# Optimization experiments

Measured on AMD Instinct MI355X. Metric: run time of the kernel, lower is better.

Reference implementation:

```python
import jax, jax.numpy as jnp
import numpy as np

ALPHA = 4.0  # spikingjelly default Sigmoid surrogate alpha
BN_EPS = 1e-5

@jax.custom_vjp
def spike(x):
    return (x >= 0.0).astype(x.dtype)

def _spike_fwd(x):
    return spike(x), x

def _spike_bwd(res, g):
    s = jax.nn.sigmoid(ALPHA * res)
    return (g * ALPHA * s * (1.0 - s),)

spike.defvjp(_spike_fwd, _spike_bwd)

def lif(x, tau=2.0, vth=1.0):
    # MultiStepLIFNode: hard reset (v_reset=0), detach_reset=True, scan over time axis 0
    def step(v, xt):
        h = v + (xt - v) / tau          # charge
        s = spike(h - vth)              # fire (surrogate grad)
        v_next = h * (1.0 - jax.lax.stop_gradient(s))  # detached hard reset to 0
        return v_next, s
    _, out = jax.lax.scan(step, jnp.zeros_like(x[0]), x)
    return out

def conv_bn(x, w, b, g, be, m, var):
    # x: [TB, C, N]; 1x1 Conv1d is a channel GEMM, then eval-mode BatchNorm1d
    y = jnp.einsum('oc,bcn->bon', w, x) + b[None, :, None]
    inv = g / jnp.sqrt(var + BN_EPS)
    return (y - m[None, :, None]) * inv[None, :, None] + be[None, :, None]

def setup_inputs() -> dict:
    key = jax.random.key(0)
    T, B, C, H, W = 4, 32, 512, 14, 14
    ks = jax.random.split(key, 32)
    d = {'x': jax.random.normal(ks[0], (T, B, C, H, W), dtype=jnp.float32)}
    scale = 1.0 / np.sqrt(C)
    i = 1
    for p in ['q', 'k', 'v', 'p']:
        d[p + '_cw'] = jax.random.normal(ks[i], (C, C), dtype=jnp.float32) * scale; i += 1
        d[p + '_cb'] = jax.random.normal(ks[i], (C,), dtype=jnp.float32) * 0.1; i += 1
        d[p + '_bg'] = jnp.ones((C,), dtype=jnp.float32)
        d[p + '_bb'] = jnp.zeros((C,), dtype=jnp.float32)
        d[p + '_bm'] = jax.random.normal(ks[i], (C,), dtype=jnp.float32) * 0.1; i += 1
        d[p + '_bv'] = jax.random.uniform(ks[i], (C,), dtype=jnp.float32, minval=0.5, maxval=1.5); i += 1
    d['push_w'] = jnp.asarray(1.0, dtype=jnp.float32)
    d['pull_w'] = jnp.asarray(1.0, dtype=jnp.float32)
    d['pp_bias'] = jnp.asarray(0.0, dtype=jnp.float32)
    return d

def reference(x,
              q_cw, q_cb, q_bg, q_bb, q_bm, q_bv,
              k_cw, k_cb, k_bg, k_bb, k_bm, k_bv,
              v_cw, v_cb, v_bg, v_bb, v_bm, v_bv,
              p_cw, p_cb, p_bg, p_bb, p_bm, p_bv,
              push_w, pull_w, pp_bias):
    T, B, C, H, W = x.shape
    N = H * W
    nh = 8
    hd = C // nh
    scale = 0.125

    xs = lif(x)                                   # head_lif, [T,B,C,H,W]
    xf = xs.reshape(T * B, C, N)
    q = conv_bn(xf, q_cw, q_cb, q_bg, q_bb, q_bm, q_bv).reshape(T, B, C, N)
    k = conv_bn(xf, k_cw, k_cb, k_bg, k_bb, k_bm, k_bv).reshape(T, B, C, N)
    v = conv_bn(xf, v_cw, v_cb, v_bg, v_bb, v_bm, v_bv).reshape(T, B, C, N)

    q_on = lif(q)
    q_off = lif(-q)

    def to_heads(t):  # [T,B,C,N] -> [T,B,nh,N,hd]
        return jnp.swapaxes(t, -1, -2).reshape(T, B, N, nh, hd).transpose(0, 1, 3, 2, 4)

    q_on_h = to_heads(q_on)
    q_off_h = to_heads(q_off)
    k_h = to_heads(lif(k))
    v_h = to_heads(lif(v))

    pw = jax.nn.softplus(push_w)
    pl = jax.nn.softplus(pull_w)
    diff = pw * q_on_h - pl * q_off_h + pp_bias   # push-pull gating
    q_pp = lif(diff)

    kv = jnp.einsum('tbhnd,tbhne->tbhde', k_h, v_h)      # k^T @ v, [T,B,h,hd,hd]
    o = jnp.einsum('tbhnd,tbhde->tbhne', q_pp, kv) * scale

    o = o.transpose(0, 1, 2, 4, 3).reshape(T, B, C, N)   # transpose(3,4) then merge heads
    o = lif(o, vth=0.5)                                   # attn_lif
    o = conv_bn(o.reshape(T * B, C, N), p_cw, p_cb, p_bg, p_bb, p_bm, p_bv)
    return o.reshape(T, B, C, H, W)
```

## Files before the change

### kernel.cpp

```cpp
#include <hip/hip_runtime.h>
#include <hip/hip_bf16.h>
#include <math.h>

typedef unsigned short u16;
typedef unsigned int   u32;

#define CC 512
#define NN 196
#define TT 4
#define BB 32
#define TBB 128
#define NHH 8
#define HD 64

#define ROWS_T  6272
#define CSTRIDE ((size_t)ROWS_T * CC)

typedef __attribute__((ext_vector_type(8))) _Float16 f16x8;
typedef __attribute__((ext_vector_type(4))) float f32x4;

#define ONE_H 0x3C00

__device__ __forceinline__ u16 h_bits(_Float16 h) { return *(u16*)&h; }
__device__ __forceinline__ float h2f(u16 u) { return (float)(*(const _Float16*)&u); }
__device__ __forceinline__ u32 pk2(u16 a, u16 b) { return (u32)a | ((u32)b << 16); }

__device__ __forceinline__ void gld16(const void* g, void* l) {
    __builtin_amdgcn_global_load_lds(
        (const __attribute__((address_space(1))) void*)g,
        (__attribute__((address_space(3))) void*)l, 16, 0, 0);
}

__global__ __launch_bounds__(256) void k_prep(
    const float* __restrict__ qw, const float* __restrict__ kw,
    const float* __restrict__ vw, const float* __restrict__ pw,
    const float* __restrict__ cb0, const float* __restrict__ bg0, const float* __restrict__ bb0,
    const float* __restrict__ bm0, const float* __restrict__ bv0,
    const float* __restrict__ cb1, const float* __restrict__ bg1, const float* __restrict__ bb1,
    const float* __restrict__ bm1, const float* __restrict__ bv1,
    const float* __restrict__ cb2, const float* __restrict__ bg2, const float* __restrict__ bb2,
    const float* __restrict__ bm2, const float* __restrict__ bv2,
    const float* __restrict__ cb3, const float* __restrict__ bg3, const float* __restrict__ bb3,
    const float* __restrict__ bm3, const float* __restrict__ bv3,
    u16* __restrict__ W2, float* __restrict__ SS, float* __restrict__ SH) {
    if (blockIdx.x < 4096) {
        size_t idx = (size_t)blockIdx.x * 256 + threadIdx.x;
        int g = (int)(idx >> 18);
        size_t rem = idx & 262143;
        const float* Ws = (g == 0) ? qw : (g == 1) ? kw : (g == 2) ? vw : pw;
        float w  = Ws[rem];
        _Float16 h0 = (fabsf(w) < 6.2e-5f) ? (_Float16)0.0f : (_Float16)w;
        float r = (w - (float)h0) * 2048.0f;
        _Float16 h1 = (_Float16)r;
        size_t base = (size_t)g * 524288 + rem;
        W2[base] = h_bits(h0); W2[base + 262144] = h_bits(h1);
        return;
    }
    int idx = (blockIdx.x - 4096) * 256 + threadIdx.x;
    int g = idx >> 9, o = idx & 511;
    const float* cb = g == 0 ? cb0 : g == 1 ? cb1 : g == 2 ? cb2 : cb3;
    const float* bg = g == 0 ? bg0 : g == 1 ? bg1 : g == 2 ? bg2 : bg3;
    const float* bb = g == 0 ? bb0 : g == 1 ? bb1 : g == 2 ? bb2 : bb3;
    const float* bm = g == 0 ? bm0 : g == 1 ? bm1 : g == 2 ? bm2 : bm3;
    const float* bv = g == 0 ? bv0 : g == 1 ? bv1 : g == 2 ? bv2 : bv3;
    float inv = bg[o] / sqrtf(bv[o] + 1e-5f);
    SS[g * 512 + o] = inv;
    SH[g * 512 + o] = (cb[o] - bm[o]) * inv + bb[o];
}

__global__ __launch_bounds__(256) void k_head_lif(const float* __restrict__ x, u16* __restrict__ XS) {
    __shared__ float T[64][65];
    const int tid = threadIdx.x;
    const int n0 = blockIdx.x * 64;
    const int b  = blockIdx.y;
    const int c_base = blockIdx.z * 64;
    const int c_l = tid >> 4;
    const int n4  = (tid & 15) * 4;
    const bool lv = (n0 + n4) < NN;
    const int n_r = tid >> 2;
    const int cq  = (tid & 3) * 16;
    const bool wv = (n0 + n_r) < NN;

    float v[4][4];
    #pragma unroll
    for (int k = 0; k < 4; ++k)
        #pragma unroll
        for (int j = 0; j < 4; ++j) v[k][j] = 0.f;

    for (int t = 0; t < TT; ++t) {
        const size_t xb = ((size_t)(t * BB + b) * CC + c_base) * NN;
        float s[4][4];
        #pragma unroll
        for (int k = 0; k < 4; ++k) {
            const int c = c_l + 16 * k;
            float4 xv = make_float4(0.f, 0.f, 0.f, 0.f);
            if (lv) xv = *(const float4*)(x + xb + (size_t)c * NN + n0 + n4);
            float xa[4] = {xv.x, xv.y, xv.z, xv.w};
            #pragma unroll
            for (int j = 0; j < 4; ++j) {
                float h = v[k][j] + (xa[j] - v[k][j]) * 0.5f;
                s[k][j] = (h >= 1.f) ? 1.f : 0.f;
                v[k][j] = (h >= 1.f) ? 0.f : h;
            }
        }
        __syncthreads();
        #pragma unroll
        for (int k = 0; k < 4; ++k)
            #pragma unroll
            for (int j = 0; j < 4; ++j) T[c_l + 16 * k][n4 + j] = s[k][j];
        __syncthreads();
        if (wv) {
            const size_t ob = ((size_t)(t * BB + b) * NN + n0 + n_r) * CC + c_base + cq;
            u16 u[16];
            #pragma unroll
            for (int m = 0; m < 16; ++m) u[m] = (T[cq + m][n_r] != 0.f) ? ONE_H : 0;
            uint4 q0 = make_uint4(pk2(u[0],u[1]),  pk2(u[2],u[3]),  pk2(u[4],u[5]),  pk2(u[6],u[7]));
            uint4 q1 = make_uint4(pk2(u[8],u[9]),  pk2(u[10],u[11]),pk2(u[12],u[13]),pk2(u[14],u[15]));
            *(uint4*)(XS + ob)     = q0;
            *(uint4*)(XS + ob + 8) = q1;
        }
        __syncthreads();
    }
}

__global__ __launch_bounds__(256) void k_gemm_qkv(const u16* __restrict__ S, const u16* __restrict__ W2,
                                                  const float* __restrict__ scale, const float* __restrict__ shift,
                                                  u16* __restrict__ QS, u16* __restrict__ KS, u16* __restrict__ VS,
                                                  const float* __restrict__ PW, const float* __restrict__ PL,
                                                  const float* __restrict__ PB) {
    __shared__ __align__(16) u16 smem[24576];
    u16* Xt  = smem;
    u16* WtF = smem + 8192;
    const int tid  = threadIdx.x;
    const int lane = tid & 63;
    const int w    = tid >> 6;
    const int bid  = blockIdx.x;
    const int work = (bid & 7) * 336 + (bid >> 3);
    const int b    = work / 84;
    const int rem  = work - b * 84;
    const int nt7  = rem / 12;
    const int gw   = rem - nt7 * 12;
    const int g    = gw >> 2;
    const int wtile = gw & 3;
    const int n0   = nt7 * 32;
    const u16* Wb = W2 + (size_t)g * 524288 + (size_t)(wtile * 128) * CC;
    const float* scl = scale + g * 512;
    const float* shf = shift + g * 512;

    const int lrow8  = lane >> 3;
    const int gchunk = ((lane & 7) ^ lrow8) * 8;
    const int l15 = lane & 15;
    const int q4  = lane >> 4;
    const int wm = (w >> 1) * 64, wn = (w & 1) * 64;

    const size_t arow0 = ((size_t)(w * 32 + b) * NN + n0) * CC;

    f32x4 acc[4][4];
    f32x4 zz = {0.f, 0.f, 0.f, 0.f};
    #pragma unroll
    for (int i = 0; i < 4; ++i)
        #pragma unroll
        for (int j = 0; j < 4; ++j) acc[i][j] = zz;

    for (int c0 = 0; c0 < CC; c0 += 64) {
        __syncthreads();
        #pragma unroll
        for (int i = 0; i < 4; ++i) {
            int p = w * 4 + i;
            gld16(S + arow0 + (size_t)(i * 8 + lrow8) * CC + c0 + gchunk, &Xt[p * 512]);
        }
        #pragma unroll
        for (int i = 0; i < 8; ++i) {
            int lin = w * 8 + i;
            int s = lin >> 4, p = lin & 15;
            gld16(Wb + (size_t)s * 262144 + (size_t)(p * 8 + lrow8) * CC + c0 + gchunk,
                  WtF + s * 8192 + p * 512);
        }
        __syncthreads();

        #pragma unroll
        for (int ks = 0; ks < 2; ++ks) {
            const int cpo = ((ks * 4 + q4) ^ (l15 & 7)) * 8;
            f16x8 sf[4], sflo[4];
            #pragma unroll
            for (int i = 0; i < 4; ++i) {
                sf[i]   = *(const f16x8*)&Xt[(wm + i * 16 + l15) * 64 + cpo];
                sflo[i] = sf[i] * (_Float16)0.00048828125f;
            }
            #pragma unroll
            for (int s = 0; s < 2; ++s) {
                f16x8 wf[4];
                #pragma unroll
                for (int i = 0; i < 4; ++i)
                    wf[i] = *(const f16x8*)&WtF[s * 8192 + (wn + i * 16 + l15) * 64 + cpo];
                #pragma unroll
                for (int mt = 0; mt < 4; ++mt)
                    #pragma unroll
                    for (int nt = 0; nt < 4; ++nt)
                        acc[mt][nt] = __builtin_amdgcn_mfma_f32_16x16x32_f16(
                            s ? sflo[mt] : sf[mt], wf[nt], acc[mt][nt], 0, 0, 0);
            }
        }
    }

    const float pwv = (g == 0) ? log1pf(expf(PW[0])) : 0.f;
    const float plv = (g == 0) ? log1pf(expf(PL[0])) : 0.f;
    const float pbv = (g == 0) ? PB[0] : 0.f;
    u16* OUT = (g == 0) ? QS : (g == 1) ? KS : VS;
    float* LY = (float*)smem;
    const int pairid = w & 1;
    const int pr  = tid >> 7;
    const int idx = tid & 127;

    #pragma unroll
    for (int cc = 0; cc < 2; ++cc) {
        __syncthreads();
        #pragma unroll
        for (int ntl = 0; ntl < 2; ++ntl) {
            const int nt = cc * 2 + ntl;
            const int o  = wtile * 128 + wn + nt * 16 + l15;
            const float sc = scl[o], sh = shf[o];
            const int col32 = ntl * 16 + l15;
            #pragma unroll
            for (int mt = 0; mt < 4; ++mt) {
                const int tr0 = wm + mt * 16 + q4 * 4;
                #pragma unroll
                for (int r = 0; r < 4; ++r)
                    LY[(pairid * 128 + tr0 + r) * 33 + col32] = acc[mt][nt][r] * sc + sh;
            }
        }
        __syncthreads();
        #pragma unroll
        for (int stp = 0; stp < 4; ++stp) {
            const int chain = stp * 128 + idx;
            const int nn  = chain >> 4;
            const int c2  = (chain & 15) * 2;
            const int n   = n0 + nn;
            const float* Lp = &LY[(pr * 128 + nn) * 33 + c2];
            float ya[4][2];
            #pragma unroll
            for (int t = 0; t < 4; ++t) {
                ya[t][0] = Lp[t * 32 * 33];
                ya[t][1] = Lp[t * 32 * 33 + 1];
            }
            if (n < NN) {
                const int ocol = wtile * 128 + pr * 64 + cc * 32 + c2;
                u32* op = (u32*)(OUT + (size_t)(b * NN + n) * CC + ocol);
                if (g == 0) {
                    float von[2] = {0.f, 0.f}, voff[2] = {0.f, 0.f}, vpp[2] = {0.f, 0.f};
                    #pragma unroll
                    for (int t = 0; t < 4; ++t) {
                        u16 sp2[2];
                        #pragma unroll
                        for (int j = 0; j < 2; ++j) {
                            float qv = ya[t][j], h;
                            h = von[j]  + ( qv - von[j] ) * 0.5f; bool s1 = (h >= 1.f); von[j]  = s1 ? 0.f : h;
                            h = voff[j] + (-qv - voff[j]) * 0.5f; bool s2 = (h >= 1.f); voff[j] = s2 ? 0.f : h;
                            float diff = pwv * (s1 ? 1.f : 0.f) - plv * (s2 ? 1.f : 0.f) + pbv;
                            h = vpp[j] + (diff - vpp[j]) * 0.5f; bool sp = (h >= 1.f); vpp[j] = sp ? 0.f : h;
                            sp2[j] = sp ? ONE_H : 0;
                        }
                        op[t * (CSTRIDE / 2)] = pk2(sp2[0], sp2[1]);
                    }
                } else {
                    float vm[2] = {0.f, 0.f};
                    #pragma unroll
                    for (int t = 0; t < 4; ++t) {
                        u16 s2[2];
                        #pragma unroll
                        for (int j = 0; j < 2; ++j) {
                            float h = vm[j] + (ya[t][j] - vm[j]) * 0.5f;
                            bool s = (h >= 1.f); vm[j] = s ? 0.f : h;
                            s2[j] = s ? ONE_H : 0;
                        }
                        op[t * (CSTRIDE / 2)] = pk2(s2[0], s2[1]);
                    }
                }
            }
        }
    }
}

__global__ __launch_bounds__(256) void k_attn(const u16* __restrict__ Q, const u16* __restrict__ K,
                                              const u16* __restrict__ V, u16* __restrict__ OS) {
    __shared__ __align__(16) u16 sm[19584];
    u16* Kt  = sm;
    u16* Vt  = sm + 8704;
    u16* Qs  = sm;
    u16* kvT = sm + 14976;

    const int tid = threadIdx.x;
    const int tb  = blockIdx.x >> 3;
    const int h   = blockIdx.x & 7;
    const size_t gb = (size_t)tb * NN * CC + (size_t)h * HD;

    const int srow = tid >> 2;
    const int sdq  = (tid & 3) * 16;

    const int lane = tid & 63;
    const int w    = tid >> 6;
    const int l15  = lane & 15;
    const int kb8  = (lane >> 4) * 8;
    const int quad = (lane >> 4) * 4;
    const int dh = (w >> 1) * 32, eh = (w & 1) * 32;

    f32x4 accA[2][2];
    f32x4 zz = {0.f, 0.f, 0.f, 0.f};
    #pragma unroll
    for (int i = 0; i < 2; ++i)
        #pragma unroll
        for (int j = 0; j < 2; ++j) accA[i][j] = zz;

    const uint4 z4 = make_uint4(0, 0, 0, 0);

    #pragma unroll
    for (int ch = 0; ch < 2; ++ch) {
        if (ch) __syncthreads();
        #pragma unroll
        for (int c = 0; c < 2; ++c) {
            int n  = ch * 128 + c * 64 + srow;
            int nl = c * 64 + srow;
            bool valid = n < NN;
            const u16* kr = K + gb + (size_t)n * CC + sdq;
            const u16* vr = V + gb + (size_t)n * CC + sdq;
            uint4 ka  = valid ? *(const uint4*)kr : z4;
            uint4 kb2 = valid ? *(const uint4*)(kr + 8) : z4;
            uint4 va  = valid ? *(const uint4*)vr : z4;
            uint4 vb2 = valid ? *(const uint4*)(vr + 8) : z4;
            u32 kwv[8] = {ka.x, ka.y, ka.z, ka.w, kb2.x, kb2.y, kb2.z, kb2.w};
            u32 vwv[8] = {va.x, va.y, va.z, va.w, vb2.x, vb2.y, vb2.z, vb2.w};
            #pragma unroll
            for (int i = 0; i < 8; ++i) {
                Kt[(sdq + 2 * i) * 136 + nl]     = (u16)(kwv[i] & 0xFFFF);
                Kt[(sdq + 2 * i + 1) * 136 + nl] = (u16)(kwv[i] >> 16);
                Vt[(sdq + 2 * i) * 136 + nl]     = (u16)(vwv[i] & 0xFFFF);
                Vt[(sdq + 2 * i + 1) * 136 + nl] = (u16)(vwv[i] >> 16);
            }
        }
        __syncthreads();
        #pragma unroll
        for (int k0 = 0; k0 < 128; k0 += 32) {
            f16x8 af[2], bv[2];
            #pragma unroll
            for (int i = 0; i < 2; ++i) {
                af[i] = *(const f16x8*)&Kt[(dh + i * 16 + l15) * 136 + k0 + kb8];
                bv[i] = *(const f16x8*)&Vt[(eh + i * 16 + l15) * 136 + k0 + kb8];
            }
            #pragma unroll
            for (int i = 0; i < 2; ++i)
                #pragma unroll
                for (int j = 0; j < 2; ++j)
                    accA[i][j] = __builtin_amdgcn_mfma_f32_16x16x32_f16(af[i], bv[j], accA[i][j], 0, 0, 0);
        }
    }
    __syncthreads();

    #pragma unroll
    for (int i = 0; i < 2; ++i)
        #pragma unroll
        for (int j = 0; j < 2; ++j)
            #pragma unroll
            for (int r = 0; r < 4; ++r) {
                int e = eh + j * 16 + l15;
                int d = dh + i * 16 + quad + r;
                _Float16 hv = (_Float16)accA[i][j][r];
                kvT[e * 72 + d] = h_bits(hv);
            }
    #pragma unroll
    for (int p = 0; p < 4; ++p) {
        int n = p * 64 + srow;
        if (n < 208) {
            if (n < NN) {
                const u16* qr = Q + gb + (size_t)n * CC + sdq;
                uint4 qa  = *(const uint4*)qr;
                uint4 qb2 = *(const uint4*)(qr + 8);
                u32 qwv[8] = {qa.x, qa.y, qa.z, qa.w, qb2.x, qb2.y, qb2.z, qb2.w};
                #pragma unroll
                for (int i = 0; i < 8; ++i) {
                    Qs[n * 72 + sdq + 2 * i]     = (u16)(qwv[i] & 0xFFFF);
                    Qs[n * 72 + sdq + 2 * i + 1] = (u16)(qwv[i] >> 16);
                }
            } else {
                #pragma unroll
                for (int i = 0; i < 16; ++i) Qs[n * 72 + sdq + i] = 0;
            }
        }
    }
    __syncthreads();

    f16x8 bq0 = *(const f16x8*)&kvT[(w * 16 + l15) * 72 + 0  + kb8];
    f16x8 bq1 = *(const f16x8*)&kvT[(w * 16 + l15) * 72 + 32 + kb8];
    u16* ob = OS + (size_t)tb * NN * CC + (size_t)h * HD + w * 16 + l15;
    #pragma unroll
    for (int nt = 0; nt < 13; ++nt) {
        f32x4 acc = zz;
        f16x8 a0 = *(const f16x8*)&Qs[(nt * 16 + l15) * 72 + 0  + kb8];
        f16x8 a1 = *(const f16x8*)&Qs[(nt * 16 + l15) * 72 + 32 + kb8];
        acc = __builtin_amdgcn_mfma_f32_16x16x32_f16(a0, bq0, acc, 0, 0, 0);
        acc = __builtin_amdgcn_mfma_f32_16x16x32_f16(a1, bq1, acc, 0, 0, 0);
        #pragma unroll
        for (int r = 0; r < 4; ++r) {
            int n = nt * 16 + quad + r;
            if (n < NN) {
                _Float16 ov = (_Float16)(acc[r] * 0.125f);
                ob[(size_t)n * CC] = h_bits(ov);
            }
        }
    }
}

__global__ __launch_bounds__(256) void k_attn_lif(uint4* __restrict__ OS) {
    const size_t idx = (size_t)blockIdx.x * 256 + threadIdx.x;
    float v[8];
    #pragma unroll
    for (int j = 0; j < 8; ++j) v[j] = 0.f;
    #pragma unroll
    for (int t = 0; t < TT; ++t) {
        const size_t o8 = idx + (size_t)t * (CSTRIDE / 8);
        uint4 d = OS[o8];
        u32 dw[4] = {d.x, d.y, d.z, d.w};
        u16 u[8];
        #pragma unroll
        for (int p = 0; p < 4; ++p) {
            #pragma unroll
            for (int hf = 0; hf < 2; ++hf) {
                int j = p * 2 + hf;
                u16 raw = hf ? (u16)(dw[p] >> 16) : (u16)(dw[p] & 0xFFFF);
                float xv = h2f(raw);
                float h = v[j] + (xv - v[j]) * 0.5f;
                bool s = (h >= 0.5f);
                v[j] = s ? 0.f : h;
                u[j] = s ? ONE_H : 0;
            }
        }
        OS[o8] = make_uint4(pk2(u[0],u[1]), pk2(u[2],u[3]), pk2(u[4],u[5]), pk2(u[6],u[7]));
    }
}

__global__ __launch_bounds__(256) void k_gemm_proj(const u16* __restrict__ S, const u16* __restrict__ W2,
                                                   const float* __restrict__ scale, const float* __restrict__ shift,
                                                   float* __restrict__ Y) {
    __shared__ __align__(16) u16 Xt[128 * 64];
    __shared__ __align__(16) u16 Wt[2][128 * 64];
    const int tid  = threadIdx.x;
    const int lane = tid & 63;
    const int w    = tid >> 6;
    const int bid  = blockIdx.x;
    const int work = (bid & 7) * 98 + (bid >> 3);
    const int ntile = work >> 2;
    const int wtile = work & 3;
    const u16* Sb = S + (size_t)ntile * 128 * CC;
    const u16* Wb = W2 + (size_t)(wtile * 128) * CC;

    const int lrow8  = lane >> 3;
    const int gchunk = ((lane & 7) ^ lrow8) * 8;
    const int l15 = lane & 15;
    const int q4  = lane >> 4;
    const int wm = (w >> 1) * 64, wn = (w & 1) * 64;

    const int tb0 = (ntile * 128) / NN;
    const int bnd = (tb0 + 1) * NN;

    f32x4 acc[4][4];
    f32x4 zz = {0.f, 0.f, 0.f, 0.f};
    #pragma unroll
    for (int i = 0; i < 4; ++i)
        #pragma unroll
        for (int j = 0; j < 4; ++j) acc[i][j] = zz;

    for (int c0 = 0; c0 < CC; c0 += 64) {
        __syncthreads();
        #pragma unroll
        for (int i = 0; i < 4; ++i) {
            int p = w * 4 + i;
            gld16(Sb + (size_t)(p * 8 + lrow8) * CC + c0 + gchunk, &Xt[p * 512]);
        }
        #pragma unroll
        for (int i = 0; i < 8; ++i) {
            int lin = w * 8 + i;
            int s = lin >> 4, p = lin & 15;
            gld16(Wb + (size_t)s * 262144 + (size_t)(p * 8 + lrow8) * CC + c0 + gchunk,
                  &Wt[s][p * 512]);
        }
        __syncthreads();

        #pragma unroll
        for (int ks = 0; ks < 2; ++ks) {
            const int cpo = ((ks * 4 + q4) ^ (l15 & 7)) * 8;
            f16x8 sf[4], sflo[4];
            #pragma unroll
            for (int i = 0; i < 4; ++i) {
                sf[i]   = *(const f16x8*)&Xt[(wn + i * 16 + l15) * 64 + cpo];
                sflo[i] = sf[i] * (_Float16)0.00048828125f;
            }
            #pragma unroll
            for (int s = 0; s < 2; ++s) {
                f16x8 wf[4];
                #pragma unroll
                for (int i = 0; i < 4; ++i)
                    wf[i] = *(const f16x8*)&Wt[s][(wm + i * 16 + l15) * 64 + cpo];
                #pragma unroll
                for (int mt = 0; mt < 4; ++mt)
                    #pragma unroll
                    for (int nt = 0; nt < 4; ++nt)
                        acc[mt][nt] = __builtin_amdgcn_mfma_f32_16x16x32_f16(
                            wf[mt], s ? sflo[nt] : sf[nt], acc[mt][nt], 0, 0, 0);
            }
        }
    }

    #pragma unroll
    for (int mt = 0; mt < 4; ++mt) {
        int o0 = wtile * 128 + wm + mt * 16 + (lane >> 4) * 4;
        #pragma unroll
        for (int nt = 0; nt < 4; ++nt) {
            int row = ntile * 128 + wn + nt * 16 + l15;
            int tb = (row >= bnd) ? tb0 + 1 : tb0;
            int n  = row - tb * NN;
            #pragma unroll
            for (int r = 0; r < 4; ++r)
                Y[((size_t)tb * CC + o0 + r) * NN + n] = acc[mt][nt][r] * scale[o0 + r] + shift[o0 + r];
        }
    }
}

extern "C" void kernel_launch(void* const* d_in, const int* in_sizes, int n_in,
                              void* d_out, int out_size, void* d_ws, size_t ws_size,
                              hipStream_t stream) {
    const float* x    = (const float*)d_in[0];
    const float* q_cw = (const float*)d_in[1];
    const float* q_cb = (const float*)d_in[2];
    const float* q_bg = (const float*)d_in[3];
    const float* q_bb = (const float*)d_in[4];
    const float* q_bm = (const float*)d_in[5];
    const float* q_bv = (const float*)d_in[6];
    const float* k_cw = (const float*)d_in[7];
    const float* k_cb = (const float*)d_in[8];
    const float* k_bg = (const float*)d_in[9];
    const float* k_bb = (const float*)d_in[10];
    const float* k_bm = (const float*)d_in[11];
    const float* k_bv = (const float*)d_in[12];
    const float* v_cw = (const float*)d_in[13];
    const float* v_cb = (const float*)d_in[14];
    const float* v_bg = (const float*)d_in[15];
    const float* v_bb = (const float*)d_in[16];
    const float* v_bm = (const float*)d_in[17];
    const float* v_bv = (const float*)d_in[18];
    const float* p_cw = (const float*)d_in[19];
    const float* p_cb = (const float*)d_in[20];
    const float* p_bg = (const float*)d_in[21];
    const float* p_bb = (const float*)d_in[22];
    const float* p_bm = (const float*)d_in[23];
    const float* p_bv = (const float*)d_in[24];
    const float* pshw = (const float*)d_in[25];
    const float* pllw = (const float*)d_in[26];
    const float* ppb  = (const float*)d_in[27];
    float* out = (float*)d_out;

    if (ws_size < (size_t)242 * 1024 * 1024) return;
    char* W = (char*)d_ws;
    u16*   XS = (u16*)W;
    u16*   QS = (u16*)(W + ((size_t)27 << 20));
    u16*   OS = (u16*)(W + ((size_t)78 << 20));
    u16*   KS = (u16*)(W + ((size_t)182 << 20));
    u16*   VS = (u16*)(W + ((size_t)208 << 20));
    u16*   W2 = (u16*)(W + ((size_t)234 << 20));
    float* SS = (float*)(W + ((size_t)238 << 20));
    float* SH = SS + 2048;

    k_prep<<<4104, 256, 0, stream>>>(q_cw, k_cw, v_cw, p_cw,
                                     q_cb, q_bg, q_bb, q_bm, q_bv,
                                     k_cb, k_bg, k_bb, k_bm, k_bv,
                                     v_cb, v_bg, v_bb, v_bm, v_bv,
                                     p_cb, p_bg, p_bb, p_bm, p_bv, W2, SS, SH);

    k_head_lif<<<dim3(4, 32, 8), 256, 0, stream>>>(x, XS);

    k_gemm_qkv<<<2688, 256, 0, stream>>>(XS, W2, SS, SH, QS, KS, VS, pshw, pllw, ppb);

    k_attn<<<TBB * NHH, 256, 0, stream>>>(QS, KS, VS, OS);
    k_attn_lif<<<1568, 256, 0, stream>>>((uint4*)OS);

    k_gemm_proj<<<784, 256, 0, stream>>>(OS, W2 + 3 * 524288, SS + 1536, SH + 1536, out);
}
```

Baseline: 332.5 us.

## Fuse attention-output LIF into attention kernel and flatten QKV GEMM row tiling

The attention kernel now loops over the four timesteps inside each block, one block per (batch, head), and keeps the attn_lif membrane state in registers. Spikes are written directly, so the separate k_attn_lif pass and its read-modify-write of OS go away. The QKV GEMM tiles rows over the flat B*N range (6272 rows, divisible by 32), which removes the padded partial n-tiles and shrinks the grid from 2688 to 2352 blocks. The LDS row strides are also padded differently (136→138, 72→74). The costs are fewer attention blocks (256 instead of 1024), serial time steps inside each block, and 52 extra float registers per thread for vO, which may reduce occupancy and parallelism.

```diff
diff --git a/kernel.cpp b/kernel.cpp
--- a/kernel.cpp
+++ b/kernel.cpp
@@ -135,14 +135,12 @@
     const int lane = tid & 63;
     const int w    = tid >> 6;
     const int bid  = blockIdx.x;
-    const int work = (bid & 7) * 336 + (bid >> 3);
-    const int b    = work / 84;
-    const int rem  = work - b * 84;
-    const int nt7  = rem / 12;
-    const int gw   = rem - nt7 * 12;
+    const int work = (bid & 7) * 294 + (bid >> 3);
+    const int rrt  = work / 12;
+    const int gw   = work - rrt * 12;
     const int g    = gw >> 2;
     const int wtile = gw & 3;
-    const int n0   = nt7 * 32;
+    const int rr0  = rrt * 32;
     const u16* Wb = W2 + (size_t)g * 524288 + (size_t)(wtile * 128) * CC;
     const float* scl = scale + g * 512;
     const float* shf = shift + g * 512;
@@ -153,7 +151,7 @@
     const int q4  = lane >> 4;
     const int wm = (w >> 1) * 64, wn = (w & 1) * 64;
 
-    const size_t arow0 = ((size_t)(w * 32 + b) * NN + n0) * CC;
+    const size_t arow0 = (size_t)w * CSTRIDE + (size_t)rr0 * CC;
 
     f32x4 acc[4][4];
     f32x4 zz = {0.f, 0.f, 0.f, 0.f};
@@ -235,7 +233,7 @@
             const int chain = stp * 128 + idx;
             const int nn  = chain >> 4;
             const int c2  = (chain & 15) * 2;
-            const int n   = n0 + nn;
+            const int rr  = rr0 + nn;
             const float* Lp = &LY[(pr * 128 + nn) * 33 + c2];
             float ya[4][2];
             #pragma unroll
@@ -243,38 +241,36 @@
                 ya[t][0] = Lp[t * 32 * 33];
                 ya[t][1] = Lp[t * 32 * 33 + 1];
             }
-            if (n < NN) {
-                const int ocol = wtile * 128 + pr * 64 + cc * 32 + c2;
-                u32* op = (u32*)(OUT + (size_t)(b * NN + n) * CC + ocol);
-                if (g == 0) {
-                    float von[2] = {0.f, 0.f}, voff[2] = {0.f, 0.f}, vpp[2] = {0.f, 0.f};
-                    #pragma unroll
-                    for (int t = 0; t < 4; ++t) {
-                        u16 sp2[2];
-                        #pragma unroll
-                        for (int j = 0; j < 2; ++j) {
-                            float qv = ya[t][j], h;
-                            h = von[j]  + ( qv - von[j] ) * 0.5f; bool s1 = (h >= 1.f); von[j]  = s1 ? 0.f : h;
-                            h = voff[j] + (-qv - voff[j]) * 0.5f; bool s2 = (h >= 1.f); voff[j] = s2 ? 0.f : h;
-                            float diff = pwv * (s1 ? 1.f : 0.f) - plv * (s2 ? 1.f : 0.f) + pbv;
-                            h = vpp[j] + (diff - vpp[j]) * 0.5f; bool sp = (h >= 1.f); vpp[j] = sp ? 0.f : h;
-                            sp2[j] = sp ? ONE_H : 0;
-                        }
-                        op[t * (CSTRIDE / 2)] = pk2(sp2[0], sp2[1]);
+            const int ocol = wtile * 128 + pr * 64 + cc * 32 + c2;
+            u32* op = (u32*)(OUT + (size_t)rr * CC + ocol);
+            if (g == 0) {
+                float von[2] = {0.f, 0.f}, voff[2] = {0.f, 0.f}, vpp[2] = {0.f, 0.f};
+                #pragma unroll
+                for (int t = 0; t < 4; ++t) {
+                    u16 sp2[2];
+                    #pragma unroll
+                    for (int j = 0; j < 2; ++j) {
+                        float qv = ya[t][j], h;
+                        h = von[j]  + ( qv - von[j] ) * 0.5f; bool s1 = (h >= 1.f); von[j]  = s1 ? 0.f : h;
+                        h = voff[j] + (-qv - voff[j]) * 0.5f; bool s2 = (h >= 1.f); voff[j] = s2 ? 0.f : h;
+                        float diff = pwv * (s1 ? 1.f : 0.f) - plv * (s2 ? 1.f : 0.f) + pbv;
+                        h = vpp[j] + (diff - vpp[j]) * 0.5f; bool sp = (h >= 1.f); vpp[j] = sp ? 0.f : h;
+                        sp2[j] = sp ? ONE_H : 0;
                     }
-                } else {
-                    float vm[2] = {0.f, 0.f};
-                    #pragma unroll
-                    for (int t = 0; t < 4; ++t) {
-                        u16 s2[2];
-                        #pragma unroll
-                        for (int j = 0; j < 2; ++j) {
-                            float h = vm[j] + (ya[t][j] - vm[j]) * 0.5f;
-                            bool s = (h >= 1.f); vm[j] = s ? 0.f : h;
-                            s2[j] = s ? ONE_H : 0;
-                        }
-                        op[t * (CSTRIDE / 2)] = pk2(s2[0], s2[1]);
+                    op[t * (CSTRIDE / 2)] = pk2(sp2[0], sp2[1]);
+                }
+            } else {
+                float vm[2] = {0.f, 0.f};
+                #pragma unroll
+                for (int t = 0; t < 4; ++t) {
+                    u16 s2[2];
+                    #pragma unroll
+                    for (int j = 0; j < 2; ++j) {
+                        float h = vm[j] + (ya[t][j] - vm[j]) * 0.5f;
+                        bool s = (h >= 1.f); vm[j] = s ? 0.f : h;
+                        s2[j] = s ? ONE_H : 0;
                     }
+                    op[t * (CSTRIDE / 2)] = pk2(s2[0], s2[1]);
                 }
             }
         }
@@ -283,16 +279,15 @@
 
 __global__ __launch_bounds__(256) void k_attn(const u16* __restrict__ Q, const u16* __restrict__ K,
                                               const u16* __restrict__ V, u16* __restrict__ OS) {
-    __shared__ __align__(16) u16 sm[19584];
+    __shared__ __align__(16) u16 sm[20128];
     u16* Kt  = sm;
-    u16* Vt  = sm + 8704;
+    u16* Vt  = sm + 8832;
     u16* Qs  = sm;
-    u16* kvT = sm + 14976;
+    u16* kvT = sm + 15392;
 
     const int tid = threadIdx.x;
-    const int tb  = blockIdx.x >> 3;
+    const int b   = blockIdx.x >> 3;
     const int h   = blockIdx.x & 7;
-    const size_t gb = (size_t)tb * NN * CC + (size_t)h * HD;
 
     const int srow = tid >> 2;
     const int sdq  = (tid & 3) * 16;
@@ -304,136 +299,123 @@
     const int quad = (lane >> 4) * 4;
     const int dh = (w >> 1) * 32, eh = (w & 1) * 32;
 
-    f32x4 accA[2][2];
     f32x4 zz = {0.f, 0.f, 0.f, 0.f};
+    const uint4 z4 = make_uint4(0, 0, 0, 0);
+
+    float vO[13][4];
     #pragma unroll
-    for (int i = 0; i < 2; ++i)
-        #pragma unroll
-        for (int j = 0; j < 2; ++j) accA[i][j] = zz;
-
-    const uint4 z4 = make_uint4(0, 0, 0, 0);
-
-    #pragma unroll
-    for (int ch = 0; ch < 2; ++ch) {
-        if (ch) __syncthreads();
-        #pragma unroll
-        for (int c = 0; c < 2; ++c) {
-            int n  = ch * 128 + c * 64 + srow;
-            int nl = c * 64 + srow;
-            bool valid = n < NN;
-            const u16* kr = K + gb + (size_t)n * CC + sdq;
-            const u16* vr = V + gb + (size_t)n * CC + sdq;
-            uint4 ka  = valid ? *(const uint4*)kr : z4;
-            uint4 kb2 = valid ? *(const uint4*)(kr + 8) : z4;
-            uint4 va  = valid ? *(const uint4*)vr : z4;
-            uint4 vb2 = valid ? *(const uint4*)(vr + 8) : z4;
-            u32 kwv[8] = {ka.x, ka.y, ka.z, ka.w, kb2.x, kb2.y, kb2.z, kb2.w};
-            u32 vwv[8] = {va.x, va.y, va.z, va.w, vb2.x, vb2.y, vb2.z, vb2.w};
-            #pragma unroll
-            for (int i = 0; i < 8; ++i) {
-                Kt[(sdq + 2 * i) * 136 + nl]     = (u16)(kwv[i] & 0xFFFF);
-                Kt[(sdq + 2 * i + 1) * 136 + nl] = (u16)(kwv[i] >> 16);
-                Vt[(sdq + 2 * i) * 136 + nl]     = (u16)(vwv[i] & 0xFFFF);
-                Vt[(sdq + 2 * i + 1) * 136 + nl] = (u16)(vwv[i] >> 16);
-            }
-        }
-        __syncthreads();
-        #pragma unroll
-        for (int k0 = 0; k0 < 128; k0 += 32) {
-            f16x8 af[2], bv[2];
-            #pragma unroll
-            for (int i = 0; i < 2; ++i) {
-                af[i] = *(const f16x8*)&Kt[(dh + i * 16 + l15) * 136 + k0 + kb8];
-                bv[i] = *(const f16x8*)&Vt[(eh + i * 16 + l15) * 136 + k0 + kb8];
-            }
-            #pragma unroll
-            for (int i = 0; i < 2; ++i)
-                #pragma unroll
-                for (int j = 0; j < 2; ++j)
-                    accA[i][j] = __builtin_amdgcn_mfma_f32_16x16x32_f16(af[i], bv[j], accA[i][j], 0, 0, 0);
-        }
-    }
-    __syncthreads();
-
-    #pragma unroll
-    for (int i = 0; i < 2; ++i)
-        #pragma unroll
-        for (int j = 0; j < 2; ++j)
+    for (int nt = 0; nt < 13; ++nt)
+        #pragma unroll
+        for (int r = 0; r < 4; ++r) vO[nt][r] = 0.f;
+
+    for (int t = 0; t < TT; ++t) {
+        const size_t gb = (size_t)(t * BB + b) * NN * CC + (size_t)h * HD;
+        __syncthreads();
+
+        f32x4 accA[2][2];
+        #pragma unroll
+        for (int i = 0; i < 2; ++i)
+            #pragma unroll
+            for (int j = 0; j < 2; ++j) accA[i][j] = zz;
+
+        #pragma unroll
+        for (int ch = 0; ch < 2; ++ch) {
+            if (ch) __syncthreads();
+            #pragma unroll
+            for (int c = 0; c < 2; ++c) {
+                int n  = ch * 128 + c * 64 + srow;
+                int nl = c * 64 + srow;
+                bool valid = n < NN;
+                const u16* kr = K + gb + (size_t)n * CC + sdq;
+                const u16* vr = V + gb + (size_t)n * CC + sdq;
+                uint4 ka  = valid ? *(const uint4*)kr : z4;
+                uint4 kb2 = valid ? *(const uint4*)(kr + 8) : z4;
+                uint4 va  = valid ? *(const uint4*)vr : z4;
+                uint4 vb2 = valid ? *(const uint4*)(vr + 8) : z4;
+                u32 kwv[8] = {ka.x, ka.y, ka.z, ka.w, kb2.x, kb2.y, kb2.z, kb2.w};
+                u32 vwv[8] = {va.x, va.y, va.z, va.w, vb2.x, vb2.y, vb2.z, vb2.w};
+                #pragma unroll
+                for (int i = 0; i < 8; ++i) {
+                    Kt[(sdq + 2 * i) * 138 + nl]     = (u16)(kwv[i] & 0xFFFF);
+                    Kt[(sdq + 2 * i + 1) * 138 + nl] = (u16)(kwv[i] >> 16);
+                    Vt[(sdq + 2 * i) * 138 + nl]     = (u16)(vwv[i] & 0xFFFF);
+                    Vt[(sdq + 2 * i + 1) * 138 + nl] = (u16)(vwv[i] >> 16);
+                }
+            }
+            __syncthreads();
+            #pragma unroll
+            for (int k0 = 0; k0 < 128; k0 += 32) {
+                f16x8 af[2], bv[2];
+                #pragma unroll
+                for (int i = 0; i < 2; ++i) {
+                    af[i] = *(const f16x8*)&Kt[(dh + i * 16 + l15) * 138 + k0 + kb8];
+                    bv[i] = *(const f16x8*)&Vt[(eh + i * 16 + l15) * 138 + k0 + kb8];
+                }
+                #pragma unroll
+                for (int i = 0; i < 2; ++i)
+                    #pragma unroll
+                    for (int j = 0; j < 2; ++j)
+                        accA[i][j] = __builtin_amdgcn_mfma_f32_16x16x32_f16(af[i], bv[j], accA[i][j], 0, 0, 0);
+            }
+        }
+        __syncthreads();
+
+        #pragma unroll
+        for (int i = 0; i < 2; ++i)
+            #pragma unroll
+            for (int j = 0; j < 2; ++j)
+                #pragma unroll
+                for (int r = 0; r < 4; ++r) {
+                    int e = eh + j * 16 + l15;
+                    int d = dh + i * 16 + quad + r;
+                    _Float16 hv = (_Float16)accA[i][j][r];
+                    kvT[e * 74 + d] = h_bits(hv);
+                }
+        #pragma unroll
+        for (int p = 0; p < 4; ++p) {
+            int n = p * 64 + srow;
+            if (n < 208) {
+                if (n < NN) {
+                    const u16* qr = Q + gb + (size_t)n * CC + sdq;
+                    uint4 qa  = *(const uint4*)qr;
+                    uint4 qb2 = *(const uint4*)(qr + 8);
+                    u32 qwv[8] = {qa.x, qa.y, qa.z, qa.w, qb2.x, qb2.y, qb2.z, qb2.w};
+                    #pragma unroll
+                    for (int i = 0; i < 8; ++i) {
+                        Qs[n * 74 + sdq + 2 * i]     = (u16)(qwv[i] & 0xFFFF);
+                        Qs[n * 74 + sdq + 2 * i + 1] = (u16)(qwv[i] >> 16);
+                    }
+                } else {
+                    #pragma unroll
+                    for (int i = 0; i < 16; ++i) Qs[n * 74 + sdq + i] = 0;
+                }
+            }
+        }
+        __syncthreads();
+
+        f16x8 bq0 = *(const f16x8*)&kvT[(w * 16 + l15) * 74 + 0  + kb8];
+        f16x8 bq1 = *(const f16x8*)&kvT[(w * 16 + l15) * 74 + 32 + kb8];
+        u16* ob = OS + (size_t)(t * BB + b) * NN * CC + (size_t)h * HD + w * 16 + l15;
+        #pragma unroll
+        for (int nt = 0; nt < 13; ++nt) {
+            f32x4 acc = zz;
+            f16x8 a0 = *(const f16x8*)&Qs[(nt * 16 + l15) * 74 + 0  + kb8];
+            f16x8 a1 = *(const f16x8*)&Qs[(nt * 16 + l15) * 74 + 32 + kb8];
+            acc = __builtin_amdgcn_mfma_f32_16x16x32_f16(a0, bq0, acc, 0, 0, 0);
+            acc = __builtin_amdgcn_mfma_f32_16x16x32_f16(a1, bq1, acc, 0, 0, 0);
             #pragma unroll
             for (int r = 0; r < 4; ++r) {
-                int e = eh + j * 16 + l15;
-                int d = dh + i * 16 + quad + r;
-                _Float16 hv = (_Float16)accA[i][j][r];
-                kvT[e * 72 + d] = h_bits(hv);
-            }
-    #pragma unroll
-    for (int p = 0; p < 4; ++p) {
-        int n = p * 64 + srow;
-        if (n < 208) {
-            if (n < NN) {
-                const u16* qr = Q + gb + (size_t)n * CC + sdq;
-                uint4 qa  = *(const uint4*)qr;
-                uint4 qb2 = *(const uint4*)(qr + 8);
-                u32 qwv[8] = {qa.x, qa.y, qa.z, qa.w, qb2.x, qb2.y, qb2.z, qb2.w};
-                #pragma unroll
-                for (int i = 0; i < 8; ++i) {
-                    Qs[n * 72 + sdq + 2 * i]     = (u16)(qwv[i] & 0xFFFF);
-                    Qs[n * 72 + sdq + 2 * i + 1] = (u16)(qwv[i] >> 16);
-                }
-            } else {
-                #pragma unroll
-                for (int i = 0; i < 16; ++i) Qs[n * 72 + sdq + i] = 0;
-            }
-        }
-    }
-    __syncthreads();
-
-    f16x8 bq0 = *(const f16x8*)&kvT[(w * 16 + l15) * 72 + 0  + kb8];
-    f16x8 bq1 = *(const f16x8*)&kvT[(w * 16 + l15) * 72 + 32 + kb8];
-    u16* ob = OS + (size_t)tb * NN * CC + (size_t)h * HD + w * 16 + l15;
-    #pragma unroll
-    for (int nt = 0; nt < 13; ++nt) {
-        f32x4 acc = zz;
-        f16x8 a0 = *(const f16x8*)&Qs[(nt * 16 + l15) * 72 + 0  + kb8];
-        f16x8 a1 = *(const f16x8*)&Qs[(nt * 16 + l15) * 72 + 32 + kb8];
-        acc = __builtin_amdgcn_mfma_f32_16x16x32_f16(a0, bq0, acc, 0, 0, 0);
-        acc = __builtin_amdgcn_mfma_f32_16x16x32_f16(a1, bq1, acc, 0, 0, 0);
-        #pragma unroll
-        for (int r = 0; r < 4; ++r) {
-            int n = nt * 16 + quad + r;
-            if (n < NN) {
-                _Float16 ov = (_Float16)(acc[r] * 0.125f);
-                ob[(size_t)n * CC] = h_bits(ov);
-            }
-        }
-    }
-}
-
-__global__ __launch_bounds__(256) void k_attn_lif(uint4* __restrict__ OS) {
-    const size_t idx = (size_t)blockIdx.x * 256 + threadIdx.x;
-    float v[8];
-    #pragma unroll
-    for (int j = 0; j < 8; ++j) v[j] = 0.f;
-    #pragma unroll
-    for (int t = 0; t < TT; ++t) {
-        const size_t o8 = idx + (size_t)t * (CSTRIDE / 8);
-        uint4 d = OS[o8];
-        u32 dw[4] = {d.x, d.y, d.z, d.w};
-        u16 u[8];
-        #pragma unroll
-        for (int p = 0; p < 4; ++p) {
-            #pragma unroll
-            for (int hf = 0; hf < 2; ++hf) {
-                int j = p * 2 + hf;
-                u16 raw = hf ? (u16)(dw[p] >> 16) : (u16)(dw[p] & 0xFFFF);
-                float xv = h2f(raw);
-                float h = v[j] + (xv - v[j]) * 0.5f;
-                bool s = (h >= 0.5f);
-                v[j] = s ? 0.f : h;
-                u[j] = s ? ONE_H : 0;
-            }
-        }
-        OS[o8] = make_uint4(pk2(u[0],u[1]), pk2(u[2],u[3]), pk2(u[4],u[5]), pk2(u[6],u[7]));
+                int n = nt * 16 + quad + r;
+                if (n < NN) {
+                    _Float16 ov = (_Float16)(acc[r] * 0.125f);
+                    float xv = (float)ov;
+                    float hl = vO[nt][r] + (xv - vO[nt][r]) * 0.5f;
+                    bool s = (hl >= 0.5f);
+                    vO[nt][r] = s ? 0.f : hl;
+                    ob[(size_t)n * CC] = s ? ONE_H : 0;
+                }
+            }
+        }
     }
 }
 
@@ -576,10 +558,9 @@
 
     k_head_lif<<<dim3(4, 32, 8), 256, 0, stream>>>(x, XS);
 
-    k_gemm_qkv<<<2688, 256, 0, stream>>>(XS, W2, SS, SH, QS, KS, VS, pshw, pllw, ppb);
-
-    k_attn<<<TBB * NHH, 256, 0, stream>>>(QS, KS, VS, OS);
-    k_attn_lif<<<1568, 256, 0, stream>>>((uint4*)OS);
+    k_gemm_qkv<<<2352, 256, 0, stream>>>(XS, W2, SS, SH, QS, KS, VS, pshw, pllw, ppb);
+
+    k_attn<<<BB * NHH, 256, 0, stream>>>(QS, KS, VS, OS);
 
     k_gemm_proj<<<784, 256, 0, stream>>>(OS, W2 + 3 * 524288, SS + 1536, SH + 1536, out);
 }
```

After: 348.6 us. +4.8%, slower.
